# Performance work log

Hardware: AMD Instinct MI355X
Metric: run time of the kernel (lower is better)

## Reference

```python
import jax, jax.numpy as jnp
import numpy as np

C = 64          # channels
N = 4096        # number of sampled coords (64x64 grid)
SPACING = (0.001, 0.001)
SHIFT = jnp.array([SPACING[0] / 2.0, SPACING[1] / 2.0], dtype=jnp.float32)  # 'nearest' mode shift


def setup_inputs() -> dict:
    key = jax.random.key(0)
    k1, k2 = jax.random.split(key)
    values = jax.random.normal(k1, (C, N), dtype=jnp.float32)
    coords = jax.random.uniform(k2, (N, 2), dtype=jnp.float32)
    return {"values": values, "coords": coords}


def reference(values, coords):
    """upsample_nn, mode='nearest', grid_mode=True, scale=4.
    values: [C, N], coords: [N, 2] -> output [C, 4N]."""
    sx, sy = SPACING
    x, y = coords[:, 0], coords[:, 1]
    # three shifted copies of the grid -> [3N, 2]
    new_coords = jnp.concatenate([
        jnp.stack([x, y + sy], axis=1),
        jnp.stack([x + sx, y], axis=1),
        jnp.stack([x + sx, y + sy], axis=1),
    ], axis=0)
    q = new_coords - SHIFT                                  # [3N, 2]
    # squared pairwise distances via expansion (argmin-equivalent to norm)
    d2 = (q * q).sum(1)[:, None] + (coords * coords).sum(1)[None, :] \
         - 2.0 * (q @ coords.T)                             # [3N, N]
    idx = jnp.argmin(d2, axis=1)                            # nearest old coord per new coord
    new_values = values[:, idx]                             # [C, 3N] irregular gather
    return jnp.concatenate([values, new_values], axis=1)    # [C, 4N]
```

## Files before the change

kernel.cpp:

```cpp
#include <hip/hip_runtime.h>


#pragma clang fp contract(off)

constexpr int   Nn    = 4096;
constexpr int   Cc    = 64;
constexpr int   NQ    = 3 * Nn;
constexpr int   GD    = 32;
constexpr int   NCELL = GD * GD;
constexpr float Rm    = 3.5e-3f;
constexpr int   QPB   = 64;
constexpr int   QBLK  = NQ / QPB;
constexpr int   NBLK  = QBLK + 64;

__global__ __launch_bounds__(256) void upsample_fused_kernel(
    const float* __restrict__ values,
    const float* __restrict__ coords,
    float* __restrict__ out)
{
#pragma clang fp contract(off)
    __shared__ int            sCnt[NCELL];
    __shared__ float2         sPts[Nn];
    __shared__ unsigned short sIds[Nn];
    __shared__ int            sBi[QPB];

    const int tid = threadIdx.x;

    if (blockIdx.x >= QBLK) {
        int b = blockIdx.x - QBLK;
        #pragma unroll
        for (int k = 0; k < 4; ++k) {
            int gi  = b * 1024 + k * 256 + tid;
            int row = gi >> 10;
            int c4  = gi & 1023;
            float4 v = reinterpret_cast<const float4*>(values)[row * 1024 + c4];
            reinterpret_cast<float4*>(out)[row * 4096 + c4] = v;
        }
        return;
    }

    const int q    = blockIdx.x * QPB + (tid & 63);
    const int isrc = q & (Nn - 1);
    float2 ci = make_float2(0.f, 0.f);
    if (tid < QPB) ci = reinterpret_cast<const float2*>(coords)[isrc];

    #pragma unroll
    for (int k = 0; k < NCELL / 256; ++k) sCnt[tid + 256 * k] = 0;

    float2 pt[16];
    int    cell[16];
    #pragma unroll
    for (int k = 0; k < 8; ++k) {
        int t4 = tid + 256 * k;
        float4 v = reinterpret_cast<const float4*>(coords)[t4];
        pt[2 * k]     = make_float2(v.x, v.y);
        pt[2 * k + 1] = make_float2(v.z, v.w);
    }
    __syncthreads();
    #pragma unroll
    for (int k = 0; k < 16; ++k) {
        int cx = min(GD - 1, (int)(pt[k].x * (float)GD));
        int cy = min(GD - 1, (int)(pt[k].y * (float)GD));
        cell[k] = cy * GD + cx;
        atomicAdd(&sCnt[cell[k]], 1);
    }
    __syncthreads();

    if (tid < 64) {
        int loc[16];
        int run = 0;
        #pragma unroll
        for (int k = 0; k < 16; ++k) { loc[k] = run; run += sCnt[tid * 16 + k]; }
        int inc = run;
        #pragma unroll
        for (int off = 1; off < 64; off <<= 1) {
            int nv = __shfl_up(inc, off, 64);
            if (tid >= off) inc += nv;
        }
        const int excl = inc - run;
        #pragma unroll
        for (int k = 0; k < 16; ++k) sCnt[tid * 16 + k] = excl + loc[k];
    }
    __syncthreads();

    #pragma unroll
    for (int k = 0; k < 16; ++k) {
        int pos = atomicAdd(&sCnt[cell[k]], 1);
        int j   = ((tid + 256 * (k >> 1)) << 1) | (k & 1);
        sPts[pos] = pt[k];
        sIds[pos] = (unsigned short)j;
    }
    __syncthreads();

    if (tid < QPB) {
        const int var = q >> 12;
        const float x = ci.x, y = ci.y;
        float qx, qy;
        if (var == 0) {
            qx = x - 0.0005f;
            qy = (y + 0.001f) - 0.0005f;
        } else if (var == 1) {
            qx = (x + 0.001f) - 0.0005f;
            qy = y - 0.0005f;
        } else {
            qx = (x + 0.001f) - 0.0005f;
            qy = (y + 0.001f) - 0.0005f;
        }
        const float qq = qx * qx + qy * qy;

        const int xlo = max(0, (int)floorf((qx - Rm) * (float)GD));
        const int xhi = min(GD - 1, (int)floorf((qx + Rm) * (float)GD));
        const int ylo = max(0, (int)floorf((qy - Rm) * (float)GD));
        const int yhi = min(GD - 1, (int)floorf((qy + Rm) * (float)GD));

        float bd = INFINITY;
        int   bi = 0x7fffffff;
        for (int cy = ylo; cy <= yhi; ++cy) {
            int cellLo = cy * GD + xlo;
            int cellHi = cy * GD + xhi;
            int s = (cellLo == 0) ? 0 : sCnt[cellLo - 1];
            int e = sCnt[cellHi];
            for (int p = s; p < e; ++p) {
                float2 c  = sPts[p];
                int    jj = sIds[p];
                float  cc = c.x * c.x + c.y * c.y;
                float  qc = __builtin_fmaf(qy, c.y, qx * c.x);
                float  d2 = (qq + cc) - (qc + qc);
                if (d2 < bd || (d2 == bd && jj < bi)) { bd = d2; bi = jj; }
            }
        }
        sBi[tid] = bi;
    }
    __syncthreads();

    {
        const int ql = tid & 63;
        const int cg = tid >> 6;
        const int bi = sBi[ql];
        const int q0 = blockIdx.x * QPB;
        #pragma unroll
        for (int k = 0; k < 16; ++k) {
            int ch = cg * 16 + k;
            out[(size_t)ch * (4 * Nn) + Nn + q0 + ql] = values[ch * Nn + bi];
        }
    }
}

extern "C" void kernel_launch(void* const* d_in, const int* in_sizes, int n_in,
                              void* d_out, int out_size, void* d_ws, size_t ws_size,
                              hipStream_t stream) {
    const float* values = (const float*)d_in[0];
    const float* coords = (const float*)d_in[1];
    float* out = (float*)d_out;
    hipLaunchKernelGGL(upsample_fused_kernel, dim3(NBLK), dim3(256), 0, stream,
                       values, coords, out);
}
```

Baseline: 13.29 us.

## Split each query's neighbor search across four lanes and fold copy into query blocks

The nearest-neighbor search previously ran on a single wavefront (64 threads) per block while the other 192 threads sat idle. Now all 256 threads work on it: four lanes share each query, stride through the candidate points, and combine their results with xor shuffles. The passthrough copy of the original values is also moved out of its 64 dedicated blocks into a grid-stride loop run by every query block, so the grid shrinks to the query blocks only. This shortens the serial per-query scan, but it adds shuffle reduction work and puts the copy traffic onto the critical path of every block.

```diff
diff --git a/kernel.cpp b/kernel.cpp
--- a/kernel.cpp
+++ b/kernel.cpp
@@ -11,7 +11,6 @@
 constexpr float Rm    = 3.5e-3f;
 constexpr int   QPB   = 64;
 constexpr int   QBLK  = NQ / QPB;
-constexpr int   NBLK  = QBLK + 64;
 
 __global__ __launch_bounds__(256) void upsample_fused_kernel(
     const float* __restrict__ values,
@@ -26,23 +25,18 @@
 
     const int tid = threadIdx.x;
 
-    if (blockIdx.x >= QBLK) {
-        int b = blockIdx.x - QBLK;
-        #pragma unroll
-        for (int k = 0; k < 4; ++k) {
-            int gi  = b * 1024 + k * 256 + tid;
-            int row = gi >> 10;
-            int c4  = gi & 1023;
-            float4 v = reinterpret_cast<const float4*>(values)[row * 1024 + c4];
-            reinterpret_cast<float4*>(out)[row * 4096 + c4] = v;
-        }
-        return;
+    for (int t = blockIdx.x * 256 + tid; t < Cc * (Nn / 4); t += QBLK * 256) {
+        int row = t >> 10;
+        int c4  = t & 1023;
+        float4 v = reinterpret_cast<const float4*>(values)[row * 1024 + c4];
+        reinterpret_cast<float4*>(out)[row * 4096 + c4] = v;
     }
 
-    const int q    = blockIdx.x * QPB + (tid & 63);
+    const int g    = tid >> 2;
+    const int l    = tid & 3;
+    const int q    = blockIdx.x * QPB + g;
     const int isrc = q & (Nn - 1);
-    float2 ci = make_float2(0.f, 0.f);
-    if (tid < QPB) ci = reinterpret_cast<const float2*>(coords)[isrc];
+    const float2 ci = reinterpret_cast<const float2*>(coords)[isrc];
 
     #pragma unroll
     for (int k = 0; k < NCELL / 256; ++k) sCnt[tid + 256 * k] = 0;
@@ -92,7 +86,7 @@
     }
     __syncthreads();
 
-    if (tid < QPB) {
+    {
         const int var = q >> 12;
         const float x = ci.x, y = ci.y;
         float qx, qy;
@@ -120,7 +114,7 @@
             int cellHi = cy * GD + xhi;
             int s = (cellLo == 0) ? 0 : sCnt[cellLo - 1];
             int e = sCnt[cellHi];
-            for (int p = s; p < e; ++p) {
+            for (int p = s + l; p < e; p += 4) {
                 float2 c  = sPts[p];
                 int    jj = sIds[p];
                 float  cc = c.x * c.x + c.y * c.y;
@@ -129,7 +123,13 @@
                 if (d2 < bd || (d2 == bd && jj < bi)) { bd = d2; bi = jj; }
             }
         }
-        sBi[tid] = bi;
+        #pragma unroll
+        for (int off = 1; off < 4; off <<= 1) {
+            float od = __shfl_xor(bd, off, 64);
+            int   oi = __shfl_xor(bi, off, 64);
+            if (od < bd || (od == bd && oi < bi)) { bd = od; bi = oi; }
+        }
+        if (l == 0) sBi[g] = bi;
     }
     __syncthreads();
 
@@ -152,6 +152,6 @@
     const float* values = (const float*)d_in[0];
     const float* coords = (const float*)d_in[1];
     float* out = (float*)d_out;
-    hipLaunchKernelGGL(upsample_fused_kernel, dim3(NBLK), dim3(256), 0, stream,
+    hipLaunchKernelGGL(upsample_fused_kernel, dim3(QBLK), dim3(256), 0, stream,
                        values, coords, out);
 }
```

After: 10.92 us. -17.8%, faster.
